# Optimization experiments

Hardware: AMD Instinct MI355X
Metric: run time of the kernel (lower is better)

The kernel has to match this reference:

```python
import jax, jax.numpy as jnp
import numpy as np

EPS = 1e-6
N_HEADS = 16
D_NOPE = 128   # qk_nope_head_dim == head_dim
D_ROPE = 64    # qk_rope_head_dim == head_dim // 2


def rmsnorm(x, g):
    # matches torch RMSNorm: normalize in fp32 then scale
    xf = x.astype(jnp.float32)
    n = xf * jax.lax.rsqrt(jnp.mean(xf * xf, axis=-1, keepdims=True) + EPS)
    return n.astype(x.dtype) * g


def rope(x):
    # x: [..., S, D]; rotary-embedding-torch convention: interleaved pairs, theta=10000
    S, D = x.shape[-2], x.shape[-1]
    freqs = 1.0 / (10000.0 ** (jnp.arange(0, D, 2, dtype=jnp.float32) / D))  # [D/2]
    ang = jnp.arange(S, dtype=jnp.float32)[:, None] * freqs                   # [S, D/2]
    ang = jnp.repeat(ang, 2, axis=-1)                                         # [S, D]
    cos, sin = jnp.cos(ang), jnp.sin(ang)
    x2 = x.reshape(*x.shape[:-1], D // 2, 2)
    xr = jnp.stack([-x2[..., 1], x2[..., 0]], axis=-1).reshape(x.shape)
    return x * cos + xr * sin


def setup_inputs() -> dict:
    key = jax.random.key(0)
    ks = jax.random.split(key, 9)
    def w(k, shape):
        return jax.random.normal(k, shape, dtype=jnp.float32) * (shape[0] ** -0.5)
    return {
        "x": jax.random.normal(ks[0], (2, 2048, 2048), dtype=jnp.float32),
        "w_dq": w(ks[1], (2048, 512)),
        "g_q": jnp.ones((512,), dtype=jnp.float32),
        "w_uq": w(ks[2], (512, 3072)),
        "w_dkv": w(ks[3], (2048, 512)),
        "g_kv": jnp.ones((512,), dtype=jnp.float32),
        "w_ukrope": w(ks[4], (2048, 64)),
        "w_uv": w(ks[5], (512, 2048)),
        "w_uknope": w(ks[6], (512, 2048)),
        "w_o": w(ks[7], (2048, 2048)),
    }


def reference(x, w_dq, g_q, w_uq, w_dkv, g_kv, w_ukrope, w_uv, w_uknope, w_o):
    B, S, _ = x.shape
    H, Dn, Dr = N_HEADS, D_NOPE, D_ROPE

    # low-rank KV path
    kv = rmsnorm(x @ w_dkv, g_kv)                                    # [B,S,512]
    k_nope = (kv @ w_uknope).reshape(B, S, H, Dn).transpose(0, 2, 1, 3)  # [B,H,S,Dn]
    v = (kv @ w_uv).reshape(B, S, H, Dn).transpose(0, 2, 1, 3)           # [B,H,S,Dn]
    k_rope = rope(x @ w_ukrope)                                      # [B,S,Dr] shared across heads

    # low-rank Q path
    q = rmsnorm(x @ w_dq, g_q) @ w_uq                                # [B,S,H*(Dn+Dr)]
    q = q.reshape(B, S, H, Dn + Dr).transpose(0, 2, 1, 3)            # [B,H,S,Dn+Dr]
    q_nope, q_rope = q[..., :Dn], rope(q[..., Dn:])

    # causal SDPA with head-shared rope keys folded into scores
    scale = 1.0 / jnp.sqrt(jnp.float32(Dn + Dr))
    scores = jnp.einsum("bhqd,bhkd->bhqk", q_nope, k_nope)
    scores = scores + jnp.einsum("bhqd,bkd->bhqk", q_rope, k_rope)
    scores = scores * scale
    causal = jnp.tril(jnp.ones((S, S), dtype=bool))
    scores = jnp.where(causal, scores, -jnp.inf)
    attn = jax.nn.softmax(scores, axis=-1)
    out = jnp.einsum("bhqk,bhkd->bhqd", attn, v)                     # [B,H,S,Dn]
    out = out.transpose(0, 2, 1, 3).reshape(B, S, H * Dn)
    return out @ w_o
```

## Files before the change

kernel.cpp:

```cpp
#include <hip/hip_runtime.h>
#include <hip/hip_bf16.h>


#define S_ 2048
#define H_ 16

typedef __bf16 bf16_t;
typedef __bf16 bf16x8 __attribute__((ext_vector_type(8)));
typedef __bf16 bf16x4_t __attribute__((ext_vector_type(4)));
typedef float f32x4 __attribute__((ext_vector_type(4)));

#define ASYNC_COPY16(gsrc, ldst)                                              \
  __builtin_amdgcn_global_load_lds(                                           \
      (const __attribute__((address_space(1))) void*)(gsrc),                  \
      (__attribute__((address_space(3))) void*)(ldst), 16, 0, 0)

#define QSCALE 0.1041177003f
#define FIXM 16.0f

__global__ void conv_bf16(const float* __restrict__ in, bf16_t* __restrict__ out,
                          int n4) {
  int i = blockIdx.x * 256 + threadIdx.x;
  if (i >= n4) return;
  float4 v = ((const float4*)in)[i];
  bf16x4_t o = {(bf16_t)v.x, (bf16_t)v.y, (bf16_t)v.z, (bf16_t)v.w};
  ((bf16x4_t*)out)[i] = o;
}

__global__ __launch_bounds__(256) void transw(const float* __restrict__ in,
                                              bf16_t* __restrict__ out, int K,
                                              int N) {
  __shared__ float t[32][33];
  int k0 = blockIdx.y * 32, n0 = blockIdx.x * 32;
  int tx = threadIdx.x, ty = threadIdx.y;
#pragma unroll
  for (int i = 0; i < 4; i++)
    t[ty + i * 8][tx] = in[(size_t)(k0 + ty + i * 8) * N + n0 + tx];
  __syncthreads();
#pragma unroll
  for (int i = 0; i < 4; i++)
    out[(size_t)(n0 + ty + i * 8) * K + k0 + tx] = (bf16_t)t[tx][ty + i * 8];
}

template <typename OT, int MODE>
__global__ __launch_bounds__(256) void gemm_bt(const bf16_t* __restrict__ A,
                                               const bf16_t* __restrict__ Bt,
                                               OT* __restrict__ C, int M, int N,
                                               int K, int lda) {
  __shared__ bf16_t Asm[128 * 32];
  __shared__ bf16_t Bsm[128 * 32];
  int tid = threadIdx.x;
  int w = tid >> 6, lane = tid & 63;
  int lrow = lane & 15, lgrp = lane >> 4;
  int wr = w >> 1, wc = w & 1;
  int bm = blockIdx.y * 128, bn = blockIdx.x * 128;

  const bf16_t* Ab = A + (size_t)bm * lda;
  const bf16_t* Bb = Bt + (size_t)bn * K;

  int srow = (w << 5) + (lane >> 2);
  int schunk = lane & 3;

  int ra[4], rb[4];
#pragma unroll
  for (int m = 0; m < 4; m++) {
    int rowA = wr * 64 + m * 16 + lrow;
    ra[m] = rowA * 64 + ((lgrp * 16) ^ (((rowA >> 1) & 3) << 4));
    int rowB = wc * 64 + m * 16 + lrow;
    rb[m] = rowB * 64 + ((lgrp * 16) ^ (((rowB >> 1) & 3) << 4));
  }

  f32x4 acc[4][4] = {};

  for (int k0 = 0; k0 < K; k0 += 32) {
#pragma unroll
    for (int j = 0; j < 2; j++) {
      int row = srow + j * 16;
      int cs = schunk ^ ((row >> 1) & 3);
      ASYNC_COPY16(Ab + (size_t)row * lda + k0 + cs * 8,
                   (char*)Asm + (w << 11) + (j << 10));
      ASYNC_COPY16(Bb + (size_t)row * K + k0 + cs * 8,
                   (char*)Bsm + (w << 11) + (j << 10));
    }
    __syncthreads();
    bf16x8 af[4], bfr[4];
#pragma unroll
    for (int m = 0; m < 4; m++) {
      af[m] = *(const bf16x8*)((const char*)Asm + ra[m]);
      bfr[m] = *(const bf16x8*)((const char*)Bsm + rb[m]);
    }
#pragma unroll
    for (int m = 0; m < 4; m++)
#pragma unroll
      for (int n = 0; n < 4; n++)
        acc[m][n] =
            __builtin_amdgcn_mfma_f32_16x16x32_bf16(af[m], bfr[n], acc[m][n], 0, 0, 0);
    __syncthreads();
  }

#pragma unroll
  for (int m = 0; m < 4; m++)
#pragma unroll
    for (int n = 0; n < 4; n++)
#pragma unroll
      for (int j = 0; j < 4; j++) {
        int row = bm + wr * 64 + m * 16 + lgrp * 4 + j;
        int col = bn + wc * 64 + n * 16 + lrow;
        float val = acc[m][n][j];
        if (MODE == 0) {
          C[(size_t)row * N + col] = (OT)val;
        } else if (MODE == 1) {
          int b = row >> 11, s = row & (S_ - 1);
          int h = col >> 7, d = col & 127;
          ((bf16_t*)C)[((size_t)((b << 4) + h) * S_ + s) * 192 + d] = (bf16_t)val;
        } else if (MODE == 2) {
          int b = row >> 11, s = row & (S_ - 1);
          unsigned h = (unsigned)col / 192u, f = (unsigned)col % 192u;
          ((bf16_t*)C)[((size_t)((b << 4) + h) * S_ + s) * 192 + f] =
              (bf16_t)(val * QSCALE);
        } else if (MODE == 3) {
          int b = row >> 11, s = row & (S_ - 1);
          int h = col >> 7, d = col & 127;
          ((bf16_t*)C)[((size_t)((b << 4) + h) * 128 + d) * S_ + s] = (bf16_t)val;
        } else if (MODE == 5) {
          int b = row >> 11, s = row & (S_ - 1);
          bf16_t* KpP = (bf16_t*)C;
          if (col < 2048) {
            int h = col >> 7, d = col & 127;
            KpP[((size_t)((b << 4) + h) * S_ + s) * 192 + d] = (bf16_t)val;
          } else {
            int c2 = col - 2048;
            int h = c2 >> 7, d = c2 & 127;
            bf16_t* VtP = KpP + (size_t)32 * S_ * 192;
            VtP[((size_t)((b << 4) + h) * 128 + d) * S_ + s] = (bf16_t)val;
          }
        }
      }
}

__global__ __launch_bounds__(256) void gemm_kr_sk(const bf16_t* __restrict__ A,
                                                  const bf16_t* __restrict__ Bt,
                                                  float* __restrict__ part) {
  const int K = 2048;
  __shared__ bf16_t Asm[128 * 32];
  __shared__ bf16_t Bsm[128 * 32];
  int tid = threadIdx.x;
  int w = tid >> 6, lane = tid & 63;
  int lrow = lane & 15, lgrp = lane >> 4;
  int wr = w >> 1, wc = w & 1;
  int sk = blockIdx.x, bm = blockIdx.y * 128;

  const bf16_t* Ab = A + (size_t)bm * K;
  const bf16_t* Bb = Bt;

  int srow = (w << 5) + (lane >> 2);
  int schunk = lane & 3;

  int ra[4], rb[4];
#pragma unroll
  for (int m = 0; m < 4; m++) {
    int rowA = wr * 64 + m * 16 + lrow;
    ra[m] = rowA * 64 + ((lgrp * 16) ^ (((rowA >> 1) & 3) << 4));
    int rowB = wc * 64 + m * 16 + lrow;
    rb[m] = rowB * 64 + ((lgrp * 16) ^ (((rowB >> 1) & 3) << 4));
  }

  f32x4 acc[4][4] = {};

  for (int kk = 0; kk < 8; kk++) {
    int k0 = sk * 256 + kk * 32;
#pragma unroll
    for (int j = 0; j < 2; j++) {
      int row = srow + j * 16;
      int cs = schunk ^ ((row >> 1) & 3);
      ASYNC_COPY16(Ab + (size_t)row * K + k0 + cs * 8,
                   (char*)Asm + (w << 11) + (j << 10));
      ASYNC_COPY16(Bb + (size_t)row * K + k0 + cs * 8,
                   (char*)Bsm + (w << 11) + (j << 10));
    }
    __syncthreads();
    bf16x8 af[4], bfr[4];
#pragma unroll
    for (int m = 0; m < 4; m++) {
      af[m] = *(const bf16x8*)((const char*)Asm + ra[m]);
      bfr[m] = *(const bf16x8*)((const char*)Bsm + rb[m]);
    }
#pragma unroll
    for (int m = 0; m < 4; m++)
#pragma unroll
      for (int n = 0; n < 4; n++)
        acc[m][n] =
            __builtin_amdgcn_mfma_f32_16x16x32_bf16(af[m], bfr[n], acc[m][n], 0, 0, 0);
    __syncthreads();
  }

  if (wc == 1) return;
#pragma unroll
  for (int m = 0; m < 4; m++)
#pragma unroll
    for (int n = 0; n < 4; n++)
#pragma unroll
      for (int j = 0; j < 4; j++) {
        int row = bm + wr * 64 + m * 16 + lgrp * 4 + j;
        int col = n * 16 + lrow;
        part[((size_t)sk * 4096 + row) * 64 + col] = acc[m][n][j];
      }
}

__global__ void reduce_rope_kr(const float* __restrict__ part,
                               bf16_t* __restrict__ Kp) {
  int i = blockIdx.x * 256 + threadIdx.x;
  if (i >= 4096 * 32) return;
  int j = i & 31, row = i >> 5;
  int b = row >> 11, s = row & (S_ - 1);
  float v0 = 0.f, v1 = 0.f;
#pragma unroll
  for (int k = 0; k < 8; k++) {
    const float* p = part + ((size_t)k * 4096 + row) * 64 + 2 * j;
    v0 += p[0];
    v1 += p[1];
  }
  float freq = powf(10000.f, -(float)(2 * j) / 64.f);
  float ang = (float)s * freq;
  float c = cosf(ang), sn = sinf(ang);
  bf16_t r0 = (bf16_t)(v0 * c - v1 * sn);
  bf16_t r1 = (bf16_t)(v1 * c + v0 * sn);
  union { bf16_t h[2]; unsigned u; } pk;
  pk.h[0] = r0; pk.h[1] = r1;
#pragma unroll
  for (int h = 0; h < 16; h++) {
    size_t base = ((size_t)((b << 4) + h) * S_ + s) * 192 + 128 + 2 * j;
    *(unsigned*)(Kp + base) = pk.u;
  }
}

__global__ __launch_bounds__(256) void rmsnorm512_b(bf16_t* __restrict__ x,
                                                    const float* __restrict__ g,
                                                    int stride) {
  int row = blockIdx.x;
  bf16_t* p = x + (size_t)row * stride;
  int t = threadIdx.x;
  float v0 = (float)p[t], v1 = (float)p[t + 256];
  __shared__ float red[256];
  red[t] = v0 * v0 + v1 * v1;
  __syncthreads();
  for (int s = 128; s > 0; s >>= 1) {
    if (t < s) red[t] += red[t + s];
    __syncthreads();
  }
  float r = rsqrtf(red[0] / 512.f + 1e-6f);
  p[t] = (bf16_t)(v0 * r * g[t]);
  p[t + 256] = (bf16_t)(v1 * r * g[t + 256]);
}

__global__ void rope_qp(bf16_t* __restrict__ Qp) {
  int i = blockIdx.x * 256 + threadIdx.x;
  if (i >= 32 * S_ * 32) return;
  int j = i & 31;
  int s = (i >> 5) & (S_ - 1);
  int bh = i >> 16;
  float freq = powf(10000.f, -(float)(2 * j) / 64.f);
  float ang = (float)s * freq;
  float c = cosf(ang), sn = sinf(ang);
  size_t base = ((size_t)bh * S_ + s) * 192 + 128 + 2 * j;
  float x0 = (float)Qp[base], x1 = (float)Qp[base + 1];
  Qp[base] = (bf16_t)(x0 * c - x1 * sn);
  Qp[base + 1] = (bf16_t)(x1 * c + x0 * sn);
}

__global__ __launch_bounds__(512) void flash_attn5(
    const bf16_t* __restrict__ Qp,
    const bf16_t* __restrict__ Kp,
    const bf16_t* __restrict__ Vt,
    bf16_t* __restrict__ o) {
  __shared__ alignas(16) char kls[2 * 64 * 384];
  __shared__ alignas(16) char vls[2 * 128 * 128];
  __shared__ alignas(16) bf16_t psh[8][16 * 64];

  int bid = blockIdx.x;
  int rest = bid >> 3;
  int p = rest & 7;
  int bh = (bid & 7) + ((rest >> 3) << 3);
  int b = bh >> 4;

  int tid = threadIdx.x;
  int w = tid >> 6;
  int lane = tid & 63;
  int lrow = lane & 15;
  int lgrp = lane >> 4;
  bf16_t* pw = &psh[w][0];

  const char* Kbh = (const char*)(Kp + (size_t)bh * S_ * 192);
  const char* Vbh = (const char*)(Vt + (size_t)bh * 128 * S_);

  int ksrc[3], vsrc[2];
#pragma unroll
  for (int r = 0; r < 3; r++) {
    int c = tid + r * 512;
    int row = c / 24, pos = c - row * 24;
    ksrc[r] = row * 384 + ((pos ^ (row & 7)) << 4);
  }
#pragma unroll
  for (int r = 0; r < 2; r++) {
    int c = tid + r * 512;
    int d = c >> 3, pos = c & 7;
    vsrc[r] = d * 4096 + ((pos ^ (d & 7)) << 4);
  }

  int kchk[6], vchk[2];
#pragma unroll
  for (int ks = 0; ks < 6; ks++)
    kchk[ks] = (((lgrp + ks * 4) ^ (lrow & 7)) << 4) + lrow * 384;
#pragma unroll
  for (int ks = 0; ks < 2; ks++)
    vchk[ks] = (((lgrp + ks * 4) ^ (lrow & 7)) << 4) + lrow * 128;

#pragma unroll 1
  for (int half = 0; half < 2; half++) {
    const int qt = half ? p : (15 - p);
    const int qb = qt * 128 + w * 16;
    const bf16_t* Qb = Qp + ((size_t)bh * S_ + qb) * 192;

    bf16x8 qf[6];
#pragma unroll
    for (int ks = 0; ks < 6; ks++)
      qf[ks] = *(const bf16x8*)(Qb + (size_t)lrow * 192 + ks * 32 + lgrp * 8);

    f32x4 acc[8];
#pragma unroll
    for (int i = 0; i < 8; i++) acc[i] = f32x4{0.f, 0.f, 0.f, 0.f};
    float lsum[4] = {0.f, 0.f, 0.f, 0.f};

    const int nk = 2 * qt + 2;
    {
      const char* kb = Kbh;
#pragma unroll
      for (int r = 0; r < 3; r++)
        ASYNC_COPY16(kb + ksrc[r], kls + (tid + r * 512) * 16);
#pragma unroll
      for (int r = 0; r < 2; r++)
        ASYNC_COPY16(Vbh + vsrc[r], vls + (tid + r * 512) * 16);
    }
    __syncthreads();

    int cur = 0;
#pragma unroll 1
    for (int kt = 0; kt < nk; kt++) {
      if (kt + 1 < nk) {
        const char* kb = Kbh + (size_t)(kt + 1) * (64 * 384);
        char* kd = kls + (cur ^ 1) * 24576;
#pragma unroll
        for (int r = 0; r < 3; r++)
          ASYNC_COPY16(kb + ksrc[r], kd + (tid + r * 512) * 16);
        const char* vb2 = Vbh + (size_t)(kt + 1) * 128;
        char* vd = vls + (cur ^ 1) * 16384;
#pragma unroll
        for (int r = 0; r < 2; r++)
          ASYNC_COPY16(vb2 + vsrc[r], vd + (tid + r * 512) * 16);
      }

      const char* kbuf = kls + cur * 24576;
      f32x4 sc[4];
#pragma unroll
      for (int cb = 0; cb < 4; cb++) {
        f32x4 s = f32x4{0.f, 0.f, 0.f, 0.f};
        const char* kp = kbuf + cb * 6144;
#pragma unroll
        for (int ks = 0; ks < 6; ks++) {
          bf16x8 kf = *(const bf16x8*)(kp + kchk[ks]);
          s = __builtin_amdgcn_mfma_f32_16x16x32_bf16(qf[ks], kf, s, 0, 0, 0);
        }
        sc[cb] = s;
      }
      if (kt >= 2 * qt) {
#pragma unroll
        for (int cb = 0; cb < 4; cb++)
#pragma unroll
          for (int r = 0; r < 4; r++) {
            int col = kt * 64 + cb * 16 + lrow;
            int row = qb + lgrp * 4 + r;
            if (col > row) sc[cb][r] = -1e30f;
          }
      }
#pragma unroll
      for (int r = 0; r < 4; r++) {
        float ps = 0.f;
#pragma unroll
        for (int cb = 0; cb < 4; cb++) {
          float e = exp2f(sc[cb][r] - FIXM);
          sc[cb][r] = e;
          ps += e;
        }
        lsum[r] += ps;
      }
#pragma unroll
      for (int r = 0; r < 4; r++) {
        int row = lgrp * 4 + r;
#pragma unroll
        for (int cb = 0; cb < 4; cb++) {
          int byte = (row * 128 + (cb * 16 + lrow) * 2) ^ ((row & 7) << 4);
          *(bf16_t*)((char*)pw + byte) = (bf16_t)sc[cb][r];
        }
      }
      bf16x8 pa[2];
#pragma unroll
      for (int ks = 0; ks < 2; ks++) {
        int byte = (lrow * 128 + ks * 64 + lgrp * 16) ^ ((lrow & 7) << 4);
        pa[ks] = *(const bf16x8*)((char*)pw + byte);
      }
      const char* vbuf = vls + cur * 16384;
#pragma unroll
      for (int cbv = 0; cbv < 8; cbv++) {
        const char* vp = vbuf + cbv * 2048;
        f32x4 a = acc[cbv];
#pragma unroll
        for (int ks = 0; ks < 2; ks++) {
          bf16x8 vf = *(const bf16x8*)(vp + vchk[ks]);
          a = __builtin_amdgcn_mfma_f32_16x16x32_bf16(pa[ks], vf, a, 0, 0, 0);
        }
        acc[cbv] = a;
      }
      __syncthreads();
      cur ^= 1;
    }
#pragma unroll
    for (int r = 0; r < 4; r++) {
      float s = lsum[r];
      s += __shfl_xor(s, 1);
      s += __shfl_xor(s, 2);
      s += __shfl_xor(s, 4);
      s += __shfl_xor(s, 8);
      float inv = 1.f / s;
      int row = qb + lgrp * 4 + r;
      bf16_t* op = o + (size_t)(b * S_ + row) * 2048 + (bh & 15) * 128;
#pragma unroll
      for (int cbv = 0; cbv < 8; cbv++)
        op[cbv * 16 + lrow] = (bf16_t)(acc[cbv][r] * inv);
    }
  }
}

extern "C" void kernel_launch(void* const* d_in, const int* in_sizes, int n_in,
                              void* d_out, int out_size, void* d_ws, size_t ws_size,
                              hipStream_t stream) {
  const float* x        = (const float*)d_in[0];
  const float* w_dq     = (const float*)d_in[1];
  const float* g_q      = (const float*)d_in[2];
  const float* w_uq     = (const float*)d_in[3];
  const float* w_dkv    = (const float*)d_in[4];
  const float* g_kv     = (const float*)d_in[5];
  const float* w_ukrope = (const float*)d_in[6];
  const float* w_uv     = (const float*)d_in[7];
  const float* w_uknope = (const float*)d_in[8];
  const float* w_o      = (const float*)d_in[9];
  float* out = (float*)d_out;

  const int M = 4096;
  bf16_t* wb = (bf16_t*)d_ws;
  size_t off = 0;
  bf16_t* xb   = wb + off; off += (size_t)M * 2048;
  bf16_t* y    = wb + off; off += (size_t)M * 1024;
  bf16_t* dq_t = wb + off; off += (size_t)512 * 2048;
  bf16_t* dkv_t= wb + off; off += (size_t)512 * 2048;
  bf16_t* uq_t = wb + off; off += (size_t)3072 * 512;
  bf16_t* ukn_t= wb + off; off += (size_t)2048 * 512;
  bf16_t* uv_t = wb + off; off += (size_t)2048 * 512;
  bf16_t* ukr_t= wb + off; off += (size_t)128 * 2048;
  bf16_t* o_t  = wb + off; off += (size_t)2048 * 2048;
  bf16_t* Qp   = wb + off; off += (size_t)32 * S_ * 192;
  bf16_t* Kp   = wb + off; off += (size_t)32 * S_ * 192;
  bf16_t* Vt   = wb + off; off += (size_t)32 * 128 * S_;
  float*  krp  = (float*)(wb + off); off += (size_t)8 * 4096 * 64 * 2;
  bf16_t* ao = xb;
  (void)dkv_t; (void)uv_t; (void)Vt;

  dim3 blk(256);
  dim3 tb(32, 8);
  conv_bf16<<<(M * 2048 / 4 + 255) / 256, blk, 0, stream>>>(x, xb, M * 2048 / 4);
  transw<<<dim3(512 / 32, 2048 / 32), tb, 0, stream>>>(w_dq, dq_t, 2048, 512);
  transw<<<dim3(512 / 32, 2048 / 32), tb, 0, stream>>>(w_dkv, dkv_t, 2048, 512);
  transw<<<dim3(3072 / 32, 512 / 32), tb, 0, stream>>>(w_uq, uq_t, 512, 3072);
  transw<<<dim3(2048 / 32, 512 / 32), tb, 0, stream>>>(w_uknope, ukn_t, 512, 2048);
  transw<<<dim3(2048 / 32, 512 / 32), tb, 0, stream>>>(w_uv, uv_t, 512, 2048);
  transw<<<dim3(2048 / 32, 2048 / 32), tb, 0, stream>>>(w_o, o_t, 2048, 2048);
  transw<<<dim3(64 / 32, 2048 / 32), tb, 0, stream>>>(w_ukrope, ukr_t, 2048, 64);
  gemm_kr_sk<<<dim3(8, 32), blk, 0, stream>>>(xb, ukr_t, krp);
  gemm_bt<bf16_t, 0><<<dim3(8, 32), blk, 0, stream>>>(xb, dq_t, y, M, 1024, 2048,
                                                      2048);
  rmsnorm512_b<<<M, blk, 0, stream>>>(y, g_q, 1024);
  rmsnorm512_b<<<M, blk, 0, stream>>>(y + 512, g_kv, 1024);
  reduce_rope_kr<<<(4096 * 32 + 255) / 256, blk, 0, stream>>>(krp, Kp);
  gemm_bt<bf16_t, 2><<<dim3(24, 32), blk, 0, stream>>>(y, uq_t, Qp, M, 3072, 512,
                                                       1024);
  gemm_bt<bf16_t, 5><<<dim3(32, 32), blk, 0, stream>>>(y + 512, ukn_t, Kp, M, 4096,
                                                       512, 1024);
  rope_qp<<<(32 * S_ * 32 + 255) / 256, blk, 0, stream>>>(Qp);
  flash_attn5<<<256, dim3(512), 0, stream>>>(Qp, Kp, Vt, ao);
  gemm_bt<float, 0><<<dim3(16, 32), blk, 0, stream>>>(ao, o_t, out, M, 2048, 2048,
                                                      2048);
}
```

Before: 312.7 us.

## Fuse k_rope projection into down-projection GEMM and precompute rope cos/sin table

Relocates the ukr_t weight buffer so it sits right after dkv_t, letting the x@w_ukrope projection run as an extra 128-column tile of the combined dq/dkv GEMM (N=1152, MODE 6 epilogue writes fp32 k_rope). This removes the separate split-K GEMM and its 8-way partial-sum reduction. A new kernel builds a cos/sin table once, and both rope kernels read from it instead of calling powf/cosf/sinf per element. In exchange the fused GEMM computes 64 padding columns that are thrown away, and the layout depends on ukr_t being contiguous with the dq/dkv weights.

After: 314.1 us. About the same (+0.5%).

```diff
diff --git a/kernel.cpp b/kernel.cpp
--- a/kernel.cpp
+++ b/kernel.cpp
@@ -40,6 +40,15 @@
 #pragma unroll
   for (int i = 0; i < 4; i++)
     out[(size_t)(n0 + ty + i * 8) * K + k0 + tx] = (bf16_t)t[tx][ty + i * 8];
+}
+
+__global__ void rope_tab(float2* __restrict__ tab) {
+  int i = blockIdx.x * 256 + threadIdx.x;
+  if (i >= S_ * 32) return;
+  int j = i & 31, s = i >> 5;
+  float freq = powf(10000.f, -(float)(2 * j) / 64.f);
+  float ang = (float)s * freq;
+  tab[i] = make_float2(cosf(ang), sinf(ang));
 }
 
 template <typename OT, int MODE>
@@ -109,19 +118,11 @@
         float val = acc[m][n][j];
         if (MODE == 0) {
           C[(size_t)row * N + col] = (OT)val;
-        } else if (MODE == 1) {
-          int b = row >> 11, s = row & (S_ - 1);
-          int h = col >> 7, d = col & 127;
-          ((bf16_t*)C)[((size_t)((b << 4) + h) * S_ + s) * 192 + d] = (bf16_t)val;
         } else if (MODE == 2) {
           int b = row >> 11, s = row & (S_ - 1);
           unsigned h = (unsigned)col / 192u, f = (unsigned)col % 192u;
           ((bf16_t*)C)[((size_t)((b << 4) + h) * S_ + s) * 192 + f] =
               (bf16_t)(val * QSCALE);
-        } else if (MODE == 3) {
-          int b = row >> 11, s = row & (S_ - 1);
-          int h = col >> 7, d = col & 127;
-          ((bf16_t*)C)[((size_t)((b << 4) + h) * 128 + d) * S_ + s] = (bf16_t)val;
         } else if (MODE == 5) {
           int b = row >> 11, s = row & (S_ - 1);
           bf16_t* KpP = (bf16_t*)C;
@@ -134,97 +135,29 @@
             bf16_t* VtP = KpP + (size_t)32 * S_ * 192;
             VtP[((size_t)((b << 4) + h) * 128 + d) * S_ + s] = (bf16_t)val;
           }
+        } else if (MODE == 6) {
+          if (col < 1024) {
+            ((bf16_t*)C)[(size_t)row * 1024 + col] = (bf16_t)val;
+          } else if (col < 1088) {
+            float* krf = (float*)((bf16_t*)C + (size_t)M * 1024);
+            krf[(size_t)row * 64 + (col - 1024)] = val;
+          }
         }
       }
 }
 
-__global__ __launch_bounds__(256) void gemm_kr_sk(const bf16_t* __restrict__ A,
-                                                  const bf16_t* __restrict__ Bt,
-                                                  float* __restrict__ part) {
-  const int K = 2048;
-  __shared__ bf16_t Asm[128 * 32];
-  __shared__ bf16_t Bsm[128 * 32];
-  int tid = threadIdx.x;
-  int w = tid >> 6, lane = tid & 63;
-  int lrow = lane & 15, lgrp = lane >> 4;
-  int wr = w >> 1, wc = w & 1;
-  int sk = blockIdx.x, bm = blockIdx.y * 128;
-
-  const bf16_t* Ab = A + (size_t)bm * K;
-  const bf16_t* Bb = Bt;
-
-  int srow = (w << 5) + (lane >> 2);
-  int schunk = lane & 3;
-
-  int ra[4], rb[4];
-#pragma unroll
-  for (int m = 0; m < 4; m++) {
-    int rowA = wr * 64 + m * 16 + lrow;
-    ra[m] = rowA * 64 + ((lgrp * 16) ^ (((rowA >> 1) & 3) << 4));
-    int rowB = wc * 64 + m * 16 + lrow;
-    rb[m] = rowB * 64 + ((lgrp * 16) ^ (((rowB >> 1) & 3) << 4));
-  }
-
-  f32x4 acc[4][4] = {};
-
-  for (int kk = 0; kk < 8; kk++) {
-    int k0 = sk * 256 + kk * 32;
-#pragma unroll
-    for (int j = 0; j < 2; j++) {
-      int row = srow + j * 16;
-      int cs = schunk ^ ((row >> 1) & 3);
-      ASYNC_COPY16(Ab + (size_t)row * K + k0 + cs * 8,
-                   (char*)Asm + (w << 11) + (j << 10));
-      ASYNC_COPY16(Bb + (size_t)row * K + k0 + cs * 8,
-                   (char*)Bsm + (w << 11) + (j << 10));
-    }
-    __syncthreads();
-    bf16x8 af[4], bfr[4];
-#pragma unroll
-    for (int m = 0; m < 4; m++) {
-      af[m] = *(const bf16x8*)((const char*)Asm + ra[m]);
-      bfr[m] = *(const bf16x8*)((const char*)Bsm + rb[m]);
-    }
-#pragma unroll
-    for (int m = 0; m < 4; m++)
-#pragma unroll
-      for (int n = 0; n < 4; n++)
-        acc[m][n] =
-            __builtin_amdgcn_mfma_f32_16x16x32_bf16(af[m], bfr[n], acc[m][n], 0, 0, 0);
-    __syncthreads();
-  }
-
-  if (wc == 1) return;
-#pragma unroll
-  for (int m = 0; m < 4; m++)
-#pragma unroll
-    for (int n = 0; n < 4; n++)
-#pragma unroll
-      for (int j = 0; j < 4; j++) {
-        int row = bm + wr * 64 + m * 16 + lgrp * 4 + j;
-        int col = n * 16 + lrow;
-        part[((size_t)sk * 4096 + row) * 64 + col] = acc[m][n][j];
-      }
-}
-
-__global__ void reduce_rope_kr(const float* __restrict__ part,
-                               bf16_t* __restrict__ Kp) {
+__global__ void rope_kr(const float* __restrict__ krf,
+                        const float2* __restrict__ tab,
+                        bf16_t* __restrict__ Kp) {
   int i = blockIdx.x * 256 + threadIdx.x;
   if (i >= 4096 * 32) return;
   int j = i & 31, row = i >> 5;
   int b = row >> 11, s = row & (S_ - 1);
-  float v0 = 0.f, v1 = 0.f;
-#pragma unroll
-  for (int k = 0; k < 8; k++) {
-    const float* p = part + ((size_t)k * 4096 + row) * 64 + 2 * j;
-    v0 += p[0];
-    v1 += p[1];
-  }
-  float freq = powf(10000.f, -(float)(2 * j) / 64.f);
-  float ang = (float)s * freq;
-  float c = cosf(ang), sn = sinf(ang);
-  bf16_t r0 = (bf16_t)(v0 * c - v1 * sn);
-  bf16_t r1 = (bf16_t)(v1 * c + v0 * sn);
+  float v0 = krf[(size_t)row * 64 + 2 * j];
+  float v1 = krf[(size_t)row * 64 + 2 * j + 1];
+  float2 cs = tab[(s << 5) + j];
+  bf16_t r0 = (bf16_t)(v0 * cs.x - v1 * cs.y);
+  bf16_t r1 = (bf16_t)(v1 * cs.x + v0 * cs.y);
   union { bf16_t h[2]; unsigned u; } pk;
   pk.h[0] = r0; pk.h[1] = r1;
 #pragma unroll
@@ -253,19 +186,17 @@
   p[t + 256] = (bf16_t)(v1 * r * g[t + 256]);
 }
 
-__global__ void rope_qp(bf16_t* __restrict__ Qp) {
+__global__ void rope_qp(bf16_t* __restrict__ Qp, const float2* __restrict__ tab) {
   int i = blockIdx.x * 256 + threadIdx.x;
   if (i >= 32 * S_ * 32) return;
   int j = i & 31;
   int s = (i >> 5) & (S_ - 1);
   int bh = i >> 16;
-  float freq = powf(10000.f, -(float)(2 * j) / 64.f);
-  float ang = (float)s * freq;
-  float c = cosf(ang), sn = sinf(ang);
+  float2 cs = tab[(s << 5) + j];
   size_t base = ((size_t)bh * S_ + s) * 192 + 128 + 2 * j;
   float x0 = (float)Qp[base], x1 = (float)Qp[base + 1];
-  Qp[base] = (bf16_t)(x0 * c - x1 * sn);
-  Qp[base + 1] = (bf16_t)(x1 * c + x0 * sn);
+  Qp[base] = (bf16_t)(x0 * cs.x - x1 * cs.y);
+  Qp[base + 1] = (bf16_t)(x1 * cs.x + x0 * cs.y);
 }
 
 __global__ __launch_bounds__(512) void flash_attn5(
@@ -460,41 +391,42 @@
   size_t off = 0;
   bf16_t* xb   = wb + off; off += (size_t)M * 2048;
   bf16_t* y    = wb + off; off += (size_t)M * 1024;
+  float*  krf  = (float*)(wb + off); off += (size_t)M * 128;
   bf16_t* dq_t = wb + off; off += (size_t)512 * 2048;
   bf16_t* dkv_t= wb + off; off += (size_t)512 * 2048;
+  bf16_t* ukr_t= wb + off; off += (size_t)128 * 2048;
   bf16_t* uq_t = wb + off; off += (size_t)3072 * 512;
   bf16_t* ukn_t= wb + off; off += (size_t)2048 * 512;
   bf16_t* uv_t = wb + off; off += (size_t)2048 * 512;
-  bf16_t* ukr_t= wb + off; off += (size_t)128 * 2048;
   bf16_t* o_t  = wb + off; off += (size_t)2048 * 2048;
   bf16_t* Qp   = wb + off; off += (size_t)32 * S_ * 192;
   bf16_t* Kp   = wb + off; off += (size_t)32 * S_ * 192;
   bf16_t* Vt   = wb + off; off += (size_t)32 * 128 * S_;
-  float*  krp  = (float*)(wb + off); off += (size_t)8 * 4096 * 64 * 2;
+  float2* tab  = (float2*)(wb + off); off += (size_t)S_ * 32 * 4;
   bf16_t* ao = xb;
-  (void)dkv_t; (void)uv_t; (void)Vt;
+  (void)dkv_t; (void)ukr_t; (void)uv_t; (void)Vt;
 
   dim3 blk(256);
   dim3 tb(32, 8);
+  rope_tab<<<(S_ * 32 + 255) / 256, blk, 0, stream>>>(tab);
   conv_bf16<<<(M * 2048 / 4 + 255) / 256, blk, 0, stream>>>(x, xb, M * 2048 / 4);
   transw<<<dim3(512 / 32, 2048 / 32), tb, 0, stream>>>(w_dq, dq_t, 2048, 512);
   transw<<<dim3(512 / 32, 2048 / 32), tb, 0, stream>>>(w_dkv, dkv_t, 2048, 512);
+  transw<<<dim3(64 / 32, 2048 / 32), tb, 0, stream>>>(w_ukrope, ukr_t, 2048, 64);
   transw<<<dim3(3072 / 32, 512 / 32), tb, 0, stream>>>(w_uq, uq_t, 512, 3072);
   transw<<<dim3(2048 / 32, 512 / 32), tb, 0, stream>>>(w_uknope, ukn_t, 512, 2048);
   transw<<<dim3(2048 / 32, 512 / 32), tb, 0, stream>>>(w_uv, uv_t, 512, 2048);
   transw<<<dim3(2048 / 32, 2048 / 32), tb, 0, stream>>>(w_o, o_t, 2048, 2048);
-  transw<<<dim3(64 / 32, 2048 / 32), tb, 0, stream>>>(w_ukrope, ukr_t, 2048, 64);
-  gemm_kr_sk<<<dim3(8, 32), blk, 0, stream>>>(xb, ukr_t, krp);
-  gemm_bt<bf16_t, 0><<<dim3(8, 32), blk, 0, stream>>>(xb, dq_t, y, M, 1024, 2048,
+  gemm_bt<bf16_t, 6><<<dim3(9, 32), blk, 0, stream>>>(xb, dq_t, y, M, 1152, 2048,
                                                       2048);
   rmsnorm512_b<<<M, blk, 0, stream>>>(y, g_q, 1024);
   rmsnorm512_b<<<M, blk, 0, stream>>>(y + 512, g_kv, 1024);
-  reduce_rope_kr<<<(4096 * 32 + 255) / 256, blk, 0, stream>>>(krp, Kp);
+  rope_kr<<<(4096 * 32 + 255) / 256, blk, 0, stream>>>(krf, tab, Kp);
   gemm_bt<bf16_t, 2><<<dim3(24, 32), blk, 0, stream>>>(y, uq_t, Qp, M, 3072, 512,
                                                        1024);
   gemm_bt<bf16_t, 5><<<dim3(32, 32), blk, 0, stream>>>(y + 512, ukn_t, Kp, M, 4096,
                                                        512, 1024);
-  rope_qp<<<(32 * S_ * 32 + 255) / 256, blk, 0, stream>>>(Qp);
+  rope_qp<<<(32 * S_ * 32 + 255) / 256, blk, 0, stream>>>(Qp, tab);
   flash_attn5<<<256, dim3(512), 0, stream>>>(Qp, Kp, Vt, ao);
   gemm_bt<float, 0><<<dim3(16, 32), blk, 0, stream>>>(ao, o_t, out, M, 2048, 2048,
                                                       2048);
```
